# Kernel tuning notes

Measured on AMD Instinct MI355X. Metric: run time of the kernel, lower is better.

Reference implementation:

```python
import jax, jax.numpy as jnp
import numpy as np
from jax import lax

STRIDE = (1, 1)
PADDING = (1, 1)


def setup_inputs() -> dict:
    key = jax.random.key(0)
    k1, k2 = jax.random.split(key)
    x = jax.random.normal(k1, (32, 128, 56, 56), dtype=jnp.float32)
    kernels = jax.random.normal(k2, (256, 128, 3, 3), dtype=jnp.float32)
    return {"x": x, "kernels": kernels}


def reference(x, kernels):
    # Equivalent to the python-loop correlation conv: NCHW input, OIHW weight,
    # cross-correlation (no kernel flip), stride/padding per module config.
    out = lax.conv_general_dilated(
        x, kernels,
        window_strides=STRIDE,
        padding=[(PADDING[0], PADDING[0]), (PADDING[1], PADDING[1])],
        dimension_numbers=("NCHW", "OIHW", "NCHW"),
    )
    return out
```

## Files before the change

### kernel.cpp

```cpp
#include <hip/hip_runtime.h>
#include <cstdint>

#define N_IMG 32
#define C_IN 128
#define H_IN 56
#define W_IN 56
#define K_OUT 256
#define HW (H_IN * W_IN)
#define M_TOTAL (N_IMG * HW)
#define XP_H 58
#define XP_W 58
#define XP_ELEMS (N_IMG * XP_H * XP_W * C_IN)
#define WT_ELEMS (9 * K_OUT * C_IN)
#define NKT 36

typedef __bf16 bf16x8 __attribute__((ext_vector_type(8)));
typedef float f32x4 __attribute__((ext_vector_type(4)));

__device__ __align__(16) unsigned short g_xp[XP_ELEMS];
__device__ __align__(16) unsigned short g_wt[WT_ELEMS];

static __device__ __forceinline__ unsigned short f2bf(float f) {
    unsigned int u = __builtin_bit_cast(unsigned int, f);
    u += 0x7fffu + ((u >> 16) & 1u);
    return (unsigned short)(u >> 16);
}

static __device__ __forceinline__ void async_copy16(const unsigned short* g, unsigned short* l) {
    auto gp = (const __attribute__((address_space(1))) unsigned int*)g;
    auto lp = (__attribute__((address_space(3))) unsigned int*)l;
    __builtin_amdgcn_global_load_lds(gp, lp, 16, 0, 0);
}

__global__ __launch_bounds__(256) void xpose_x(const float* __restrict__ x) {
    __shared__ float tile[C_IN * 57];
    const int h = blockIdx.x;
    const int n = blockIdx.y;
    const int tid = threadIdx.x;

    if (tid < 32) {
        int col = (tid >> 4) * (XP_W - 1);
        int q = tid & 15;
        uint4* dst = (uint4*)(g_xp + ((size_t)(n * XP_H + h + 1) * XP_W + col) * C_IN) + q;
        *dst = uint4{0u, 0u, 0u, 0u};
    }
    if (h == 0 || h == H_IN - 1) {
        int hp = (h == 0) ? 0 : XP_H - 1;
        uint4* base = (uint4*)(g_xp + ((size_t)(n * XP_H + hp) * XP_W) * C_IN);
        for (int q = tid; q < (XP_W * C_IN) / 8; q += 256) base[q] = uint4{0u, 0u, 0u, 0u};
    }

#pragma unroll
    for (int i = 0; i < 28; i++) {
        int e = i * 256 + tid;
        int c = e / 56;
        int w = e - c * 56;
        tile[c * 57 + w] = x[((n * C_IN + c) * H_IN + h) * W_IN + w];
    }
    __syncthreads();
    unsigned int* outp = (unsigned int*)g_xp;
#pragma unroll
    for (int i = 0; i < 14; i++) {
        int u = i * 256 + tid;
        int w = u >> 6;
        int cp = u & 63;
        float a = tile[(2 * cp) * 57 + w];
        float b = tile[(2 * cp + 1) * 57 + w];
        unsigned int pk = (unsigned int)f2bf(a) | ((unsigned int)f2bf(b) << 16);
        int idx = ((n * XP_H + h + 1) * XP_W + (w + 1)) * C_IN + 2 * cp;
        outp[idx >> 1] = pk;
    }
}

__global__ __launch_bounds__(256) void xpose_w(const float* __restrict__ w) {
    int e = blockIdx.x * 256 + threadIdx.x;
    int rr = e >> 15;
    int rem = e & 32767;
    int k = rem >> 7;
    int c = rem & 127;
    g_wt[e] = f2bf(w[(k * C_IN + c) * 9 + rr]);
}

__global__ __launch_bounds__(512, 4) void conv_main(float* __restrict__ out) {
    __shared__ __align__(16) unsigned short As[2][8192];
    __shared__ __align__(16) unsigned short Bs[2][4096];
    const unsigned short* __restrict__ xp = g_xp;
    const unsigned short* __restrict__ wt = g_wt;

    const int tid = threadIdx.x;
    const int wave = tid >> 6, lane = tid & 63;
    const int lr = lane & 15, lq = lane >> 4;
    const int wmL = (wave >> 1) * 64;
    const int wnL = (wave & 1) * 64;

    const int bid = blockIdx.x;
    const int g = (bid & 7) * 98 + (bid >> 3);
    const int m0 = (g >> 1) * 256;
    const int k0 = (g & 1) * 128;

    int a_src[2], lds_a[2];
#pragma unroll
    for (int j = 0; j < 2; j++) {
        const int u = j * 512 + tid;
        const int row = u >> 2, seg = u & 3;
        const int sw = (seg ^ (row & 3)) * 8;
        int p = m0 + row;
        int n = p / HW;
        int rem = p - n * HW;
        int h = rem / W_IN;
        int w = rem - h * W_IN;
        a_src[j] = ((n * XP_H + h) * XP_W + w) * C_IN + sw;
        lds_a[j] = (j * 512 + wave * 64) * 8;
    }
    const int brow_s = tid >> 2, bseg = tid & 3;
    const int b_src = (k0 + brow_s) * C_IN + (bseg ^ (brow_s & 3)) * 8;
    const int lds_b = wave * 64 * 8;

    const int csw = (lq ^ (lr & 3)) * 8;

    auto stage_tile = [&](int kt, int nb) {
        const int rs = kt >> 2;
        const int r = (rs * 11) >> 5;
        const int sc = rs - r * 3;
        const int aoff = (r * XP_W + sc) * C_IN + (kt & 3) * 32;
        const int boff = rs * (K_OUT * C_IN) + (kt & 3) * 32;
#pragma unroll
        for (int j = 0; j < 2; j++)
            async_copy16(xp + a_src[j] + aoff, &As[nb][lds_a[j]]);
        async_copy16(wt + b_src + boff, &Bs[nb][lds_b]);
    };

    f32x4 acc[4][4];
#pragma unroll
    for (int mi = 0; mi < 4; mi++)
#pragma unroll
        for (int ni = 0; ni < 4; ni++) acc[mi][ni] = f32x4{0.f, 0.f, 0.f, 0.f};

    stage_tile(0, 0);
    stage_tile(1, 1);
    asm volatile("s_waitcnt vmcnt(3)" ::: "memory");
    __builtin_amdgcn_s_barrier();
    asm volatile("" ::: "memory");

#pragma unroll 2
    for (int t = 0; t < NKT; ++t) {
        const int b = t & 1;
        bf16x8 af[4], bfv[4];

#pragma unroll
        for (int mi = 0; mi < 4; mi++)
            af[mi] = *(const bf16x8*)(&As[b][(wmL + mi * 16 + lr) * 32 + csw]);
#pragma unroll
        for (int ni = 0; ni < 4; ni++)
            bfv[ni] = *(const bf16x8*)(&Bs[b][(wnL + ni * 16 + lr) * 32 + csw]);
        __builtin_amdgcn_s_barrier();
        asm volatile("s_waitcnt lgkmcnt(0)" ::: "memory");
        __builtin_amdgcn_sched_barrier(0);
        __builtin_amdgcn_s_setprio(1);
#pragma unroll
        for (int mi = 0; mi < 4; mi++)
#pragma unroll
            for (int ni = 0; ni < 2; ni++)
                acc[mi][ni] = __builtin_amdgcn_mfma_f32_16x16x32_bf16(
                    af[mi], bfv[ni], acc[mi][ni], 0, 0, 0);
        __builtin_amdgcn_s_setprio(0);
        __builtin_amdgcn_s_barrier();
        asm volatile("" ::: "memory");

        if (t + 2 < NKT) stage_tile(t + 2, b);
        __builtin_amdgcn_s_setprio(1);
#pragma unroll
        for (int mi = 0; mi < 4; mi++)
#pragma unroll
            for (int ni = 2; ni < 4; ni++)
                acc[mi][ni] = __builtin_amdgcn_mfma_f32_16x16x32_bf16(
                    af[mi], bfv[ni], acc[mi][ni], 0, 0, 0);
        __builtin_amdgcn_s_setprio(0);
        if (t + 2 < NKT) {
            asm volatile("s_waitcnt vmcnt(3)" ::: "memory");
        } else {
            asm volatile("s_waitcnt vmcnt(0)" ::: "memory");
        }
        __builtin_amdgcn_s_barrier();
        asm volatile("" ::: "memory");
    }

#pragma unroll
    for (int mi = 0; mi < 4; mi++) {
        int p = m0 + wmL + mi * 16 + lq * 4;
        int n = p / HW;
        int off = p - n * HW;
#pragma unroll
        for (int ni = 0; ni < 4; ni++) {
            int k = k0 + wnL + ni * 16 + lr;
            *(f32x4*)(out + (n * K_OUT + k) * HW + off) = acc[mi][ni];
        }
    }
}

extern "C" void kernel_launch(void* const* d_in, const int* in_sizes, int n_in,
                              void* d_out, int out_size, void* d_ws, size_t ws_size,
                              hipStream_t stream) {
    const float* x = (const float*)d_in[0];
    const float* w = (const float*)d_in[1];
    float* out = (float*)d_out;

    hipLaunchKernelGGL(xpose_x, dim3(H_IN, N_IMG), dim3(256), 0, stream, x);
    hipLaunchKernelGGL(xpose_w, dim3(WT_ELEMS / 256), dim3(256), 0, stream, w);
    hipLaunchKernelGGL(conv_main, dim3((M_TOTAL / 256) * (K_OUT / 128)), dim3(512), 0, stream, out);
}
```

Baseline: 230.8 us.

## Triple-buffer LDS tiles and change swizzle to reduce barriers and bank conflicts

```diff
diff --git a/kernel.cpp b/kernel.cpp
--- a/kernel.cpp
+++ b/kernel.cpp
@@ -82,8 +82,8 @@
 }
 
 __global__ __launch_bounds__(512, 4) void conv_main(float* __restrict__ out) {
-    __shared__ __align__(16) unsigned short As[2][8192];
-    __shared__ __align__(16) unsigned short Bs[2][4096];
+    __shared__ __align__(16) unsigned short As[3][8192];
+    __shared__ __align__(16) unsigned short Bs[3][4096];
     const unsigned short* __restrict__ xp = g_xp;
     const unsigned short* __restrict__ wt = g_wt;
 
@@ -101,9 +101,9 @@
     int a_src[2], lds_a[2];
 #pragma unroll
     for (int j = 0; j < 2; j++) {
-        const int u = j * 512 + tid;
-        const int row = u >> 2, seg = u & 3;
-        const int sw = (seg ^ (row & 3)) * 8;
+        const int su = j * 512 + tid;
+        const int row = su >> 2, seg = su & 3;
+        const int sw = (seg ^ ((row >> 1) & 3)) * 8;
         int p = m0 + row;
         int n = p / HW;
         int rem = p - n * HW;
@@ -113,10 +113,10 @@
         lds_a[j] = (j * 512 + wave * 64) * 8;
     }
     const int brow_s = tid >> 2, bseg = tid & 3;
-    const int b_src = (k0 + brow_s) * C_IN + (bseg ^ (brow_s & 3)) * 8;
+    const int b_src = (k0 + brow_s) * C_IN + (bseg ^ ((brow_s >> 1) & 3)) * 8;
     const int lds_b = wave * 64 * 8;
 
-    const int csw = (lq ^ (lr & 3)) * 8;
+    const int csw = (lq ^ ((lr >> 1) & 3)) * 8;
 
     auto stage_tile = [&](int kt, int nb) {
         const int rs = kt >> 2;
@@ -142,47 +142,37 @@
     __builtin_amdgcn_s_barrier();
     asm volatile("" ::: "memory");
 
-#pragma unroll 2
-    for (int t = 0; t < NKT; ++t) {
-        const int b = t & 1;
-        bf16x8 af[4], bfv[4];
-
-#pragma unroll
-        for (int mi = 0; mi < 4; mi++)
-            af[mi] = *(const bf16x8*)(&As[b][(wmL + mi * 16 + lr) * 32 + csw]);
-#pragma unroll
-        for (int ni = 0; ni < 4; ni++)
-            bfv[ni] = *(const bf16x8*)(&Bs[b][(wnL + ni * 16 + lr) * 32 + csw]);
-        __builtin_amdgcn_s_barrier();
-        asm volatile("s_waitcnt lgkmcnt(0)" ::: "memory");
-        __builtin_amdgcn_sched_barrier(0);
-        __builtin_amdgcn_s_setprio(1);
-#pragma unroll
-        for (int mi = 0; mi < 4; mi++)
-#pragma unroll
-            for (int ni = 0; ni < 2; ni++)
-                acc[mi][ni] = __builtin_amdgcn_mfma_f32_16x16x32_bf16(
-                    af[mi], bfv[ni], acc[mi][ni], 0, 0, 0);
-        __builtin_amdgcn_s_setprio(0);
-        __builtin_amdgcn_s_barrier();
-        asm volatile("" ::: "memory");
-
-        if (t + 2 < NKT) stage_tile(t + 2, b);
-        __builtin_amdgcn_s_setprio(1);
-#pragma unroll
-        for (int mi = 0; mi < 4; mi++)
-#pragma unroll
-            for (int ni = 2; ni < 4; ni++)
-                acc[mi][ni] = __builtin_amdgcn_mfma_f32_16x16x32_bf16(
-                    af[mi], bfv[ni], acc[mi][ni], 0, 0, 0);
-        __builtin_amdgcn_s_setprio(0);
-        if (t + 2 < NKT) {
-            asm volatile("s_waitcnt vmcnt(3)" ::: "memory");
-        } else {
-            asm volatile("s_waitcnt vmcnt(0)" ::: "memory");
+    for (int tt = 0; tt < NKT / 3; ++tt) {
+#pragma unroll
+        for (int u = 0; u < 3; u++) {
+            const int t = tt * 3 + u;
+            if (t + 2 < NKT) stage_tile(t + 2, (u + 2) % 3);
+
+            bf16x8 af[4], bfv[4];
+#pragma unroll
+            for (int mi = 0; mi < 4; mi++)
+                af[mi] = *(const bf16x8*)(&As[u][(wmL + mi * 16 + lr) * 32 + csw]);
+#pragma unroll
+            for (int ni = 0; ni < 4; ni++)
+                bfv[ni] = *(const bf16x8*)(&Bs[u][(wnL + ni * 16 + lr) * 32 + csw]);
+            asm volatile("s_waitcnt lgkmcnt(0)" ::: "memory");
+            __builtin_amdgcn_sched_barrier(0);
+            __builtin_amdgcn_s_setprio(1);
+#pragma unroll
+            for (int mi = 0; mi < 4; mi++)
+#pragma unroll
+                for (int ni = 0; ni < 4; ni++)
+                    acc[mi][ni] = __builtin_amdgcn_mfma_f32_16x16x32_bf16(
+                        af[mi], bfv[ni], acc[mi][ni], 0, 0, 0);
+            __builtin_amdgcn_s_setprio(0);
+            if (t + 2 < NKT) {
+                asm volatile("s_waitcnt vmcnt(3)" ::: "memory");
+            } else {
+                asm volatile("s_waitcnt vmcnt(0)" ::: "memory");
+            }
+            __builtin_amdgcn_s_barrier();
+            asm volatile("" ::: "memory");
         }
-        __builtin_amdgcn_s_barrier();
-        asm volatile("" ::: "memory");
     }
 
 #pragma unroll
```

Measured after the change: 239.5 us. 3.8% more time.
